# Kernel optimization log

Hardware: AMD Instinct MI355X
Metric: run time of the kernel (lower is better)

The kernel has to match this reference:

```python
import jax, jax.numpy as jnp
import numpy as np

N_HEAD = 16  # head_dim = C // N_HEAD = 128


def setup_inputs() -> dict:
    key = jax.random.key(0)
    k1, k2, k3 = jax.random.split(key, 3)
    B, T, C = 2, 2048, 2048
    x = jax.random.normal(k1, (B, T, C), dtype=jnp.float32)
    # c_attn: Linear(C, 3*C), no bias; stored as (in, out) for x @ W
    w_attn = jax.random.normal(k2, (C, 3 * C), dtype=jnp.float32) * (1.0 / np.sqrt(C))
    # c_proj: Linear(C, C), no bias
    w_proj = jax.random.normal(k3, (C, C), dtype=jnp.float32) * (1.0 / np.sqrt(C))
    return {"x": x, "w_attn": w_attn, "w_proj": w_proj}


def reference(x, w_attn, w_proj):
    B, T, C = x.shape
    H = N_HEAD
    D = C // H  # head dimension
    qkv = x @ w_attn                      # [B, T, 3C]
    q, k, v = jnp.split(qkv, 3, axis=-1)  # each [B, T, C]
    # [B, T, C] -> [B, H, T, D]
    q = q.reshape(B, T, H, D).transpose(0, 2, 1, 3)
    k = k.reshape(B, T, H, D).transpose(0, 2, 1, 3)
    v = v.reshape(B, T, H, D).transpose(0, 2, 1, 3)
    scale = 1.0 / np.sqrt(D).astype(np.float32)
    att = jnp.einsum('bhqd,bhkd->bhqk', q, k) * scale  # [B, H, T, T]
    causal = jnp.tril(jnp.ones((T, T), dtype=bool))
    att = jnp.where(causal[None, None, :, :], att, jnp.float32(-jnp.inf))
    att = jax.nn.softmax(att, axis=-1)
    y = jnp.einsum('bhqk,bhkd->bhqd', att, v)  # [B, H, T, D]
    y = y.transpose(0, 2, 1, 3).reshape(B, T, C)
    # all_reduce is identity with number_of_workers=1; dropout=0 (eval)
    return y @ w_proj
```

## Files before the change

### kernel.cpp

```cpp
#include <hip/hip_runtime.h>
#include <hip/hip_bf16.h>
#include <stdint.h>

#define TLEN 2048
#define CDIM 2048
#define BDIM 2
#define HDIM 16
#define DHEAD 128
#define QROW ((size_t)(2 * CDIM))

typedef __bf16 bf16x8 __attribute__((ext_vector_type(8)));
typedef float f32x4 __attribute__((ext_vector_type(4)));

__device__ __forceinline__ uint16_t f32_to_bf16(float f) {
    uint32_t u = __builtin_bit_cast(uint32_t, f);
    uint32_t r = (u + 0x7FFFu + ((u >> 16) & 1u)) >> 16;
    return (uint16_t)r;
}
__device__ __forceinline__ float bf16_to_f32(uint32_t h) {
    uint32_t u = h << 16;
    return __builtin_bit_cast(float, u);
}

__device__ __forceinline__ void gload_lds16(const uint16_t* g, uint16_t* l) {
    __builtin_amdgcn_global_load_lds(
        (const __attribute__((address_space(1))) uint32_t*)g,
        (__attribute__((address_space(3))) uint32_t*)l, 16, 0, 0);
}

__global__ void cvt_f32_bf16(const float* __restrict__ in, uint16_t* __restrict__ out, int n) {
    int i = (blockIdx.x * blockDim.x + threadIdx.x) * 4;
    if (i + 3 < n) {
        float4 f = *reinterpret_cast<const float4*>(in + i);
        ushort4 o;
        o.x = f32_to_bf16(f.x);
        o.y = f32_to_bf16(f.y);
        o.z = f32_to_bf16(f.z);
        o.w = f32_to_bf16(f.w);
        *reinterpret_cast<ushort4*>(out + i) = o;
    }
}

__global__ __launch_bounds__(256) void transpose_cvt(const float* __restrict__ in,
                                                     uint16_t* __restrict__ out,
                                                     int R, int Cc) {
    __shared__ uint16_t tile[64][65];
    int c0 = blockIdx.x * 64;
    int r0 = blockIdx.y * 64;
    int tc = threadIdx.x & 63;
    int t4 = threadIdx.x >> 6;
    for (int rr = t4; rr < 64; rr += 4) {
        tile[rr][tc] = f32_to_bf16(in[(size_t)(r0 + rr) * Cc + c0 + tc]);
    }
    __syncthreads();
    int wr = threadIdx.x & 63;
    for (int cc = t4; cc < 64; cc += 4) {
        out[(size_t)(c0 + cc) * R + r0 + wr] = tile[wr][cc];
    }
}


#define RD8(P, OFF) (*reinterpret_cast<const bf16x8*>((P) + (OFF)))

#define PH_RDA(BA, MB)                                              \
    _Pragma("unroll") for (int mi = 0; mi < 4; mi++) {              \
        af[mi][0] = RD8(BA, rdAo + ((MB) + mi) * 1024 + kblk0);     \
        af[mi][1] = RD8(BA, rdAo + ((MB) + mi) * 1024 + kblk1);     \
    }

#define PH_RDB(BB, NIB)                                                  \
    _Pragma("unroll") for (int ni = 0; ni < 2; ni++) {                   \
        bf[(NIB) + ni][0] = RD8(BB, rdBo + ((NIB) + ni) * 1024 + kblk0); \
        bf[(NIB) + ni][1] = RD8(BB, rdBo + ((NIB) + ni) * 1024 + kblk1); \
    }

#define PH_MFMA(MB, NIB)                                                        \
    __builtin_amdgcn_s_barrier();                                               \
    asm volatile("s_waitcnt lgkmcnt(0)" ::: "memory");                          \
    __builtin_amdgcn_s_setprio(1);                                              \
    _Pragma("unroll") for (int mi = 0; mi < 4; mi++)                            \
    _Pragma("unroll") for (int ni = 0; ni < 2; ni++) {                          \
        acc[(MB) + mi][(NIB) + ni] = __builtin_amdgcn_mfma_f32_16x16x32_bf16(   \
            af[mi][0], bf[(NIB) + ni][0], acc[(MB) + mi][(NIB) + ni], 0, 0, 0); \
        acc[(MB) + mi][(NIB) + ni] = __builtin_amdgcn_mfma_f32_16x16x32_bf16(   \
            af[mi][1], bf[(NIB) + ni][1], acc[(MB) + mi][(NIB) + ni], 0, 0, 0); \
    }                                                                           \
    __builtin_amdgcn_s_setprio(0);                                              \
    __builtin_amdgcn_s_barrier();                                               \
    __builtin_amdgcn_sched_barrier(0);

#define TILE(S, T)                                           \
    {                                                        \
        const int k0 = (T) * 64;                             \
        const uint16_t* bA = As + ((S) + wrow) * 8192;       \
        const uint16_t* bB = Bs + ((S) + bsel) * 8192;       \
        PH_RDA(bA, 0)                                        \
        PH_RDB(bB, 0)                                        \
        PH_MFMA(0, 0)                                        \
        PH_RDB(bB, 2)                                        \
        PH_MFMA(0, 2)                                        \
        PH_RDA(bA, 4)                                        \
        if ((T) + 2 < nt) {                                  \
            stB((S), 0, k0 + 128);                           \
            stB((S), 1, k0 + 128);                           \
        }                                                    \
        PH_MFMA(4, 2)                                        \
        if ((T) + 2 < nt) {                                  \
            stA((S), 0, k0 + 128);                           \
            stA((S), 1, k0 + 128);                           \
            asm volatile("s_waitcnt vmcnt(8)" ::: "memory"); \
        } else {                                             \
            asm volatile("s_waitcnt vmcnt(0)" ::: "memory"); \
        }                                                    \
        PH_MFMA(4, 0)                                        \
    }

template <int MODE>
__global__ __launch_bounds__(512, 2) void gemm_bf16_256(const uint16_t* __restrict__ A,
                                                        const uint16_t* __restrict__ Bt,
                                                        void* __restrict__ Cp,
                                                        uint16_t* __restrict__ vt,
                                                        int M, int N, int K, int xm) {
    __shared__ __align__(16) uint16_t lds[65536];
    uint16_t* const As = lds;
    uint16_t* const Bs = lds + 32768;

    const int tid = threadIdx.x;
    const int wave = tid >> 6;
    const int lane = tid & 63;
    const int l15 = lane & 15;
    const int quad = lane >> 4;
    const int wrow = wave >> 2;
    const int wcol = wave & 3;
    const int bsel = wcol >> 1;

    const int gm = gridDim.y, gn = gridDim.x;
    const int flat = blockIdx.y * gn + blockIdx.x;
    const int xcd = flat & 7;
    const int j = flat >> 3;
    const int xn = 8 / xm;
    const int RM = gm / xm;
    const int RN = gn / xn;
    const int m_blk = (xcd / xn) * RM + (j % RM);
    const int n_blk = (xcd % xn) * RN + (j / RM);
    const int m0 = m_blk * 256;
    const int n0 = n_blk * 256;

    const int srow = wave * 8 + (lane >> 3);
    const int scol = ((lane & 7) ^ (lane >> 3)) * 8;
    const uint16_t* Ag = A + (size_t)(m0 + srow) * K + scol;
    const uint16_t* Bg = Bt + (size_t)(n0 + srow) * K + scol;
    const int ldsoff = wave * 512;

    const int rdAo = l15 * 64;
    const int rdBo = ((wcol & 1) * 64 + l15) * 64;
    const int kblk0 = (quad ^ (l15 & 7)) * 8;
    const int kblk1 = ((4 + quad) ^ (l15 & 7)) * 8;

    const int nt = K >> 6;
    f32x4 acc[8][4] = {};
    bf16x8 af[4][2], bf[4][2];

    auto stA = [&](int sb, int h, int kk) {
        const uint16_t* s = Ag + (size_t)(h * 128) * K + kk;
        uint16_t* d = As + (sb + h) * 8192 + ldsoff;
        gload_lds16(s, d);
        gload_lds16(s + (size_t)64 * K, d + 4096);
    };
    auto stB = [&](int sb, int h, int kk) {
        const uint16_t* s = Bg + (size_t)(h * 128) * K + kk;
        uint16_t* d = Bs + (sb + h) * 8192 + ldsoff;
        gload_lds16(s, d);
        gload_lds16(s + (size_t)64 * K, d + 4096);
    };

    stB(0, 0, 0);
    stB(0, 1, 0);
    stA(0, 0, 0);
    stA(0, 1, 0);
    stB(2, 0, 64);
    stB(2, 1, 64);
    stA(2, 0, 64);
    stA(2, 1, 64);
    asm volatile("s_waitcnt vmcnt(8)" ::: "memory");
    __builtin_amdgcn_s_barrier();
    __builtin_amdgcn_sched_barrier(0);

    for (int t = 0; t < nt; t += 2) {
        TILE(0, t)
        TILE(2, t + 1)
    }

    const bool vmode = (MODE == 2) && (n0 >= 2 * CDIM);
#pragma unroll
    for (int mi = 0; mi < 8; mi++)
#pragma unroll
        for (int ni = 0; ni < 4; ni++) {
            if (vmode) {
                int col = n0 + wcol * 64 + ni * 16 + l15;
                int vcol = col - 2 * CDIM;
                int hh = vcol >> 7, d = vcol & 127;
                int rowm = m0 + wrow * 128 + mi * 16 + quad * 4;
                int bb = rowm >> 11, tt = rowm & 2047;
                uint32_t lo = (uint32_t)f32_to_bf16(acc[mi][ni][0]) |
                              ((uint32_t)f32_to_bf16(acc[mi][ni][1]) << 16);
                uint32_t hi = (uint32_t)f32_to_bf16(acc[mi][ni][2]) |
                              ((uint32_t)f32_to_bf16(acc[mi][ni][3]) << 16);
                *reinterpret_cast<uint2*>(
                    vt + ((size_t)((bb * HDIM + hh) * DHEAD + d)) * TLEN + tt) =
                    make_uint2(lo, hi);
            } else {
#pragma unroll
                for (int r = 0; r < 4; r++) {
                    int row = m0 + wrow * 128 + mi * 16 + quad * 4 + r;
                    int col = n0 + wcol * 64 + ni * 16 + l15;
                    float v = acc[mi][ni][r];
                    if (MODE == 2)
                        ((uint16_t*)Cp)[(size_t)row * (2 * CDIM) + col] = f32_to_bf16(v);
                    else if (MODE == 1)
                        ((uint16_t*)Cp)[(size_t)row * N + col] = f32_to_bf16(v);
                    else
                        ((float*)Cp)[(size_t)row * N + col] = v;
                }
            }
        }
}

#define ATT_C1 0.12751743f
#define ATT_C2 17.3123405f

__global__ __launch_bounds__(256) void attn_mfma3(const uint16_t* __restrict__ qkv,
                                                  const uint16_t* __restrict__ vtg,
                                                  uint16_t* __restrict__ y) {
    __shared__ __align__(16) uint16_t Ks[64 * 128];
    __shared__ __align__(16) uint16_t Vts[128 * 64];
    __shared__ __align__(16) uint16_t Ps[4][32 * 72];

    const int tid = threadIdx.x;
    const int wave = tid >> 6;
    const int lane = tid & 63;
    const int l15 = lane & 15;
    const int quad = lane >> 4;
    const int h = blockIdx.y;
    const int b = blockIdx.z;
    const int qblk = (int)gridDim.x - 1 - (int)blockIdx.x;
    const int qbase = qblk * 128 + wave * 32;
    const int kmax = qbase + 31;

    const uint16_t* kg = qkv + (size_t)b * TLEN * QROW + CDIM + h * DHEAD;
    const uint16_t* vg = vtg + (size_t)(b * HDIM + h) * DHEAD * TLEN;
    uint16_t* PsW = Ps[wave];

    int koff[4], voff[4];
#pragma unroll
    for (int i = 0; i < 4; i++) {
        int Lb = (wave * 4 + i) * 64 + lane;
        int key = Lb >> 4;
        int ck = (Lb & 15) ^ (key & 15);
        koff[i] = key * (int)QROW + ck * 8;
        int d = Lb >> 3;
        int cv = (Lb & 7) ^ (d & 7);
        voff[i] = d * TLEN + cv * 8;
    }

    bf16x8 qfrag[2][4];
#pragma unroll
    for (int m = 0; m < 2; m++) {
        const uint16_t* qp =
            qkv + (size_t)(b * TLEN + qbase + m * 16 + l15) * QROW + h * DHEAD + quad * 8;
#pragma unroll
        for (int kc = 0; kc < 4; kc++)
            qfrag[m][kc] = *reinterpret_cast<const bf16x8*>(qp + kc * 32);
    }

    f32x4 oacc[2][8] = {};
    float psum[2] = {0.f, 0.f};

    const int diagT = qblk * 2 + (wave >> 1);
    const int ntiles = qblk * 2 + 2;

    for (int t = 0; t < ntiles; t++) {
        const int j0 = t * 64;
        if (t > 0) __syncthreads();
        {
            const uint16_t* kj = kg + (size_t)j0 * QROW;
            const uint16_t* vj = vg + j0;
#pragma unroll
            for (int i = 0; i < 4; i++) {
                gload_lds16(kj + koff[i], Ks + (wave * 4 + i) * 512);
                gload_lds16(vj + voff[i], Vts + (wave * 4 + i) * 512);
            }
        }
        __syncthreads();
        if (t > diagT) continue;

        const bool masked = (t == diagT);
        const int n0max = masked ? ((kmax - j0) >> 4) : 3;

        f32x4 st[4][2];
#pragma unroll
        for (int n0 = 0; n0 < 4; n0++) {
            if (masked && n0 > n0max) continue;
            bf16x8 kf[4];
#pragma unroll
            for (int kc = 0; kc < 4; kc++) {
                int cpr = (kc * 4 + quad) ^ l15;
                kf[kc] = *reinterpret_cast<const bf16x8*>(
                    Ks + (n0 * 16 + l15) * 128 + cpr * 8);
            }
#pragma unroll
            for (int m = 0; m < 2; m++) {
                f32x4 acc = {};
#pragma unroll
                for (int kc = 0; kc < 4; kc++)
                    acc = __builtin_amdgcn_mfma_f32_16x16x32_bf16(
                        kf[kc], qfrag[m][kc], acc, 0, 0, 0);
                st[n0][m] = acc;
            }
        }

#pragma unroll
        for (int n0 = 0; n0 < 4; n0++) {
            if (masked && n0 > n0max) continue;
#pragma unroll
            for (int m = 0; m < 2; m++) {
                uint32_t pk0, pk1;
                float pv[4];
#pragma unroll
                for (int r = 0; r < 4; r++) {
                    float p = exp2f(st[n0][m][r] * ATT_C1 - ATT_C2);
                    if (masked) {
                        int key = j0 + n0 * 16 + quad * 4 + r;
                        int q = qbase + m * 16 + l15;
                        if (key > q) p = 0.f;
                    }
                    uint32_t pb = f32_to_bf16(p);
                    pv[r] = bf16_to_f32(pb);
                    if (r == 0) pk0 = pb;
                    else if (r == 1) pk0 |= pb << 16;
                    else if (r == 2) pk1 = pb;
                    else pk1 |= pb << 16;
                }
                psum[m] += (pv[0] + pv[1]) + (pv[2] + pv[3]);
                *reinterpret_cast<uint2*>(PsW + (m * 16 + l15) * 72 + n0 * 16 + quad * 4) =
                    make_uint2(pk0, pk1);
            }
        }

        const int kcend = masked ? (((kmax - j0) >> 5) + 1) : 2;
#pragma unroll
        for (int kc = 0; kc < 2; kc++) {
            if (kc >= kcend) continue;
            bf16x8 pf[2];
#pragma unroll
            for (int m = 0; m < 2; m++)
                pf[m] = *reinterpret_cast<const bf16x8*>(
                    PsW + (m * 16 + l15) * 72 + kc * 32 + quad * 8);
#pragma unroll
            for (int n0 = 0; n0 < 8; n0++) {
                int cpr = (kc * 4 + quad) ^ (l15 & 7);
                bf16x8 vf = *reinterpret_cast<const bf16x8*>(
                    Vts + (n0 * 16 + l15) * 64 + cpr * 8);
#pragma unroll
                for (int m = 0; m < 2; m++)
                    oacc[m][n0] = __builtin_amdgcn_mfma_f32_16x16x32_bf16(
                        pf[m], vf, oacc[m][n0], 0, 0, 0);
            }
        }
    }

#pragma unroll
    for (int m = 0; m < 2; m++) {
        float s = psum[m];
        s += __shfl_xor(s, 16);
        s += __shfl_xor(s, 32);
        psum[m] = 1.0f / s;
    }
    uint16_t* ybase = y + (size_t)(b * TLEN + qbase) * CDIM + h * DHEAD;
#pragma unroll
    for (int m = 0; m < 2; m++)
#pragma unroll
        for (int r = 0; r < 4; r++) {
            float inv = __shfl(psum[m], quad * 4 + r);
#pragma unroll
            for (int n0 = 0; n0 < 8; n0++)
                ybase[(size_t)(m * 16 + quad * 4 + r) * CDIM + n0 * 16 + l15] =
                    f32_to_bf16(oacc[m][n0][r] * inv);
        }
}

extern "C" void kernel_launch(void* const* d_in, const int* in_sizes, int n_in,
                              void* d_out, int out_size, void* d_ws, size_t ws_size,
                              hipStream_t stream) {
    const float* x = (const float*)d_in[0];
    const float* w_attn = (const float*)d_in[1];
    const float* w_proj = (const float*)d_in[2];
    float* out = (float*)d_out;

    const int M = BDIM * TLEN;
    const int K = CDIM;
    const int N3 = 3 * CDIM;

    char* ws = (char*)d_ws;
    uint16_t* xb = (uint16_t*)(ws);
    uint16_t* waT = (uint16_t*)(ws + 16777216);
    uint16_t* wpT = (uint16_t*)(ws + 41943040);
    uint16_t* qkp = (uint16_t*)(ws + 50331648);
    uint16_t* vtb = (uint16_t*)(ws + 83886080);
    uint16_t* yb = (uint16_t*)(ws + 100663296);

    cvt_f32_bf16<<<(M * K / 4 + 255) / 256, 256, 0, stream>>>(x, xb, M * K);
    transpose_cvt<<<dim3(N3 / 64, K / 64), 256, 0, stream>>>(w_attn, waT, K, N3);
    transpose_cvt<<<dim3(K / 64, K / 64), 256, 0, stream>>>(w_proj, wpT, K, K);
    gemm_bf16_256<2><<<dim3(N3 / 256, M / 256), 512, 0, stream>>>(xb, waT, (void*)qkp, vtb, M, N3, K, 2);
    attn_mfma3<<<dim3(TLEN / 128, HDIM, BDIM), 256, 0, stream>>>(qkp, vtb, yb);
    gemm_bf16_256<0><<<dim3(K / 256, M / 256), 512, 0, stream>>>(yb, wpT, (void*)out, nullptr, M, K, K, 4);
}
```

Before: 434.8 us.

## Software-pipeline LDS fragment reads across GEMM tile phases with double-buffered registers

Splits the A and B fragment registers into separate low/high and ping-pong buffers so that LDS reads for the next phase, and for the next k-tile, are issued before the current MFMA block runs. Partial lgkmcnt waits replace full drains, so LDS latency can overlap with matrix math. The global-load wait is also moved so that next-tile fragments can be read early. This raises register pressure and makes the waitcnt accounting fragile under a 512-thread, 2-blocks-per-CU launch bound.

```diff
diff --git a/kernel.cpp b/kernel.cpp
--- a/kernel.cpp
+++ b/kernel.cpp
@@ -62,57 +62,76 @@
 
 #define RD8(P, OFF) (*reinterpret_cast<const bf16x8*>((P) + (OFF)))
 
-#define PH_RDA(BA, MB)                                              \
-    _Pragma("unroll") for (int mi = 0; mi < 4; mi++) {              \
-        af[mi][0] = RD8(BA, rdAo + ((MB) + mi) * 1024 + kblk0);     \
-        af[mi][1] = RD8(BA, rdAo + ((MB) + mi) * 1024 + kblk1);     \
-    }
-
-#define PH_RDB(BB, NIB)                                                  \
-    _Pragma("unroll") for (int ni = 0; ni < 2; ni++) {                   \
-        bf[(NIB) + ni][0] = RD8(BB, rdBo + ((NIB) + ni) * 1024 + kblk0); \
-        bf[(NIB) + ni][1] = RD8(BB, rdBo + ((NIB) + ni) * 1024 + kblk1); \
-    }
-
-#define PH_MFMA(MB, NIB)                                                        \
-    __builtin_amdgcn_s_barrier();                                               \
-    asm volatile("s_waitcnt lgkmcnt(0)" ::: "memory");                          \
-    __builtin_amdgcn_s_setprio(1);                                              \
-    _Pragma("unroll") for (int mi = 0; mi < 4; mi++)                            \
-    _Pragma("unroll") for (int ni = 0; ni < 2; ni++) {                          \
-        acc[(MB) + mi][(NIB) + ni] = __builtin_amdgcn_mfma_f32_16x16x32_bf16(   \
-            af[mi][0], bf[(NIB) + ni][0], acc[(MB) + mi][(NIB) + ni], 0, 0, 0); \
-        acc[(MB) + mi][(NIB) + ni] = __builtin_amdgcn_mfma_f32_16x16x32_bf16(   \
-            af[mi][1], bf[(NIB) + ni][1], acc[(MB) + mi][(NIB) + ni], 0, 0, 0); \
-    }                                                                           \
-    __builtin_amdgcn_s_setprio(0);                                              \
-    __builtin_amdgcn_s_barrier();                                               \
+#define RDA(DST, P, MB)                                         \
+    _Pragma("unroll") for (int mi = 0; mi < 4; mi++) {          \
+        DST[mi][0] = RD8(P, rdAo + ((MB) + mi) * 1024 + kblk0); \
+        DST[mi][1] = RD8(P, rdAo + ((MB) + mi) * 1024 + kblk1); \
+    }
+
+#define RDB(DST, P, NB)                                         \
+    _Pragma("unroll") for (int ni = 0; ni < 2; ni++) {          \
+        DST[ni][0] = RD8(P, rdBo + ((NB) + ni) * 1024 + kblk0); \
+        DST[ni][1] = RD8(P, rdBo + ((NB) + ni) * 1024 + kblk1); \
+    }
+
+#define MFMA8(AF, BF, MB, NIB)                                                \
+    _Pragma("unroll") for (int mi = 0; mi < 4; mi++)                          \
+    _Pragma("unroll") for (int ni = 0; ni < 2; ni++) {                        \
+        acc[(MB) + mi][(NIB) + ni] = __builtin_amdgcn_mfma_f32_16x16x32_bf16( \
+            AF[mi][0], BF[ni][0], acc[(MB) + mi][(NIB) + ni], 0, 0, 0);       \
+        acc[(MB) + mi][(NIB) + ni] = __builtin_amdgcn_mfma_f32_16x16x32_bf16( \
+            AF[mi][1], BF[ni][1], acc[(MB) + mi][(NIB) + ni], 0, 0, 0);       \
+    }
+
+#define PHASE(LGN, AF, BF, MB, NIB)                           \
+    __builtin_amdgcn_s_barrier();                             \
+    asm volatile("s_waitcnt lgkmcnt(" #LGN ")" ::: "memory"); \
+    __builtin_amdgcn_sched_barrier(0);                        \
+    __builtin_amdgcn_s_setprio(1);                            \
+    MFMA8(AF, BF, MB, NIB)                                    \
+    __builtin_amdgcn_s_setprio(0);                            \
+    __builtin_amdgcn_s_barrier();                             \
     __builtin_amdgcn_sched_barrier(0);
 
-#define TILE(S, T)                                           \
-    {                                                        \
-        const int k0 = (T) * 64;                             \
-        const uint16_t* bA = As + ((S) + wrow) * 8192;       \
-        const uint16_t* bB = Bs + ((S) + bsel) * 8192;       \
-        PH_RDA(bA, 0)                                        \
-        PH_RDB(bB, 0)                                        \
-        PH_MFMA(0, 0)                                        \
-        PH_RDB(bB, 2)                                        \
-        PH_MFMA(0, 2)                                        \
-        PH_RDA(bA, 4)                                        \
-        if ((T) + 2 < nt) {                                  \
-            stB((S), 0, k0 + 128);                           \
-            stB((S), 1, k0 + 128);                           \
-        }                                                    \
-        PH_MFMA(4, 2)                                        \
-        if ((T) + 2 < nt) {                                  \
-            stA((S), 0, k0 + 128);                           \
-            stA((S), 1, k0 + 128);                           \
-            asm volatile("s_waitcnt vmcnt(8)" ::: "memory"); \
-        } else {                                             \
-            asm volatile("s_waitcnt vmcnt(0)" ::: "memory"); \
-        }                                                    \
-        PH_MFMA(4, 0)                                        \
+#define TILE(S, T, BFL, BFH)                                  \
+    {                                                         \
+        const int k0 = (T) * 64;                              \
+        const uint16_t* pA = As + ((S) + wrow) * 8192;        \
+        const uint16_t* pB = Bs + ((S) + bsel) * 8192;        \
+        const uint16_t* pAn = As + (((S) ^ 2) + wrow) * 8192; \
+        const uint16_t* pBn = Bs + (((S) ^ 2) + bsel) * 8192; \
+                               \
+        RDB(BFH, pB, 2)                                       \
+        PHASE(4, aL, BFL, 0, 0)                               \
+                               \
+        RDA(aH, pA, 4)                                        \
+        PHASE(8, aL, BFH, 0, 2)                               \
+                               \
+        if ((T) + 2 < nt) {                                   \
+            stB((S), 0, k0 + 128);                            \
+            stB((S), 1, k0 + 128);                            \
+        }                                                     \
+        PHASE(0, aH, BFH, 4, 2)                               \
+          \
+        if ((T) + 2 < nt) {                                   \
+            asm volatile("s_waitcnt vmcnt(4)" ::: "memory");  \
+            stA((S), 0, k0 + 128);                            \
+            stA((S), 1, k0 + 128);                            \
+        } else if ((T) + 1 < nt) {                            \
+            asm volatile("s_waitcnt vmcnt(0)" ::: "memory");  \
+        }                                                     \
+        __builtin_amdgcn_s_barrier();                         \
+        if ((T) + 1 < nt) {                                   \
+            RDA(aL, pAn, 0)                                   \
+            RDB(BFH, pBn, 0)                                  \
+        }                                                     \
+        asm volatile("s_waitcnt lgkmcnt(12)" ::: "memory");   \
+        __builtin_amdgcn_sched_barrier(0);                    \
+        __builtin_amdgcn_s_setprio(1);                        \
+        MFMA8(aH, BFL, 4, 0)                                  \
+        __builtin_amdgcn_s_setprio(0);                        \
+        __builtin_amdgcn_s_barrier();                         \
+        __builtin_amdgcn_sched_barrier(0);                    \
     }
 
 template <int MODE>
@@ -159,7 +178,7 @@
 
     const int nt = K >> 6;
     f32x4 acc[8][4] = {};
-    bf16x8 af[4][2], bf[4][2];
+    bf16x8 aL[4][2], aH[4][2], b0[2][2], b1[2][2];
 
     auto stA = [&](int sb, int h, int kk) {
         const uint16_t* s = Ag + (size_t)(h * 128) * K + kk;
@@ -185,10 +204,12 @@
     asm volatile("s_waitcnt vmcnt(8)" ::: "memory");
     __builtin_amdgcn_s_barrier();
     __builtin_amdgcn_sched_barrier(0);
+    RDA(aL, (As + wrow * 8192), 0)
+    RDB(b0, (Bs + bsel * 8192), 0)
 
     for (int t = 0; t < nt; t += 2) {
-        TILE(0, t)
-        TILE(2, t + 1)
+        TILE(0, t, b0, b1)
+        TILE(2, t + 1, b1, b0)
     }
 
     const bool vmode = (MODE == 2) && (n0 >= 2 * CDIM);
```

After: 599.6 us. +37.9%, slower.

## Restructure GEMM tile schedule into two larger MFMA phases with fewer barriers

Applied to the files above, without the earlier changes.

Replaces the four-phase per-tile schedule, each phase with its own barrier pair and lgkmcnt(0) wait, with a two-phase schedule. All four B fragments are loaded once per tile and each phase issues 32 MFMAs over two A row groups, with the global-to-LDS prefetch stores issued between barriers. The goal is to cut barrier and LDS-wait overhead and to hand the matrix cores longer uninterrupted runs. In exchange the changed wait counts and barrier placement must still prevent LDS read/write races, and the final tile skips its vmcnt wait.

```diff
diff --git a/kernel.cpp b/kernel.cpp
--- a/kernel.cpp
+++ b/kernel.cpp
@@ -62,57 +62,61 @@
 
 #define RD8(P, OFF) (*reinterpret_cast<const bf16x8*>((P) + (OFF)))
 
-#define PH_RDA(BA, MB)                                              \
-    _Pragma("unroll") for (int mi = 0; mi < 4; mi++) {              \
-        af[mi][0] = RD8(BA, rdAo + ((MB) + mi) * 1024 + kblk0);     \
-        af[mi][1] = RD8(BA, rdAo + ((MB) + mi) * 1024 + kblk1);     \
-    }
-
-#define PH_RDB(BB, NIB)                                                  \
-    _Pragma("unroll") for (int ni = 0; ni < 2; ni++) {                   \
-        bf[(NIB) + ni][0] = RD8(BB, rdBo + ((NIB) + ni) * 1024 + kblk0); \
-        bf[(NIB) + ni][1] = RD8(BB, rdBo + ((NIB) + ni) * 1024 + kblk1); \
-    }
-
-#define PH_MFMA(MB, NIB)                                                        \
-    __builtin_amdgcn_s_barrier();                                               \
-    asm volatile("s_waitcnt lgkmcnt(0)" ::: "memory");                          \
-    __builtin_amdgcn_s_setprio(1);                                              \
-    _Pragma("unroll") for (int mi = 0; mi < 4; mi++)                            \
-    _Pragma("unroll") for (int ni = 0; ni < 2; ni++) {                          \
-        acc[(MB) + mi][(NIB) + ni] = __builtin_amdgcn_mfma_f32_16x16x32_bf16(   \
-            af[mi][0], bf[(NIB) + ni][0], acc[(MB) + mi][(NIB) + ni], 0, 0, 0); \
-        acc[(MB) + mi][(NIB) + ni] = __builtin_amdgcn_mfma_f32_16x16x32_bf16(   \
-            af[mi][1], bf[(NIB) + ni][1], acc[(MB) + mi][(NIB) + ni], 0, 0, 0); \
-    }                                                                           \
-    __builtin_amdgcn_s_setprio(0);                                              \
-    __builtin_amdgcn_s_barrier();                                               \
-    __builtin_amdgcn_sched_barrier(0);
+#define RDA(DST, P, MB)                                         \
+    _Pragma("unroll") for (int mi = 0; mi < 4; mi++) {          \
+        DST[mi][0] = RD8(P, rdAo + ((MB) + mi) * 1024 + kblk0); \
+        DST[mi][1] = RD8(P, rdAo + ((MB) + mi) * 1024 + kblk1); \
+    }
+
+#define RDB4(DST, P)                                        \
+    _Pragma("unroll") for (int ni = 0; ni < 4; ni++) {      \
+        DST[ni][0] = RD8(P, rdBo + ni * 1024 + kblk0);      \
+        DST[ni][1] = RD8(P, rdBo + ni * 1024 + kblk1);      \
+    }
+
+#define MFMA32(MB)                                                    \
+    _Pragma("unroll") for (int kk = 0; kk < 2; kk++)                  \
+    _Pragma("unroll") for (int mi = 0; mi < 4; mi++)                  \
+    _Pragma("unroll") for (int ni = 0; ni < 4; ni++)                  \
+        acc[(MB) + mi][ni] = __builtin_amdgcn_mfma_f32_16x16x32_bf16( \
+            aA[mi][kk], bB[ni][kk], acc[(MB) + mi][ni], 0, 0, 0);
 
 #define TILE(S, T)                                           \
     {                                                        \
         const int k0 = (T) * 64;                             \
-        const uint16_t* bA = As + ((S) + wrow) * 8192;       \
-        const uint16_t* bB = Bs + ((S) + bsel) * 8192;       \
-        PH_RDA(bA, 0)                                        \
-        PH_RDB(bB, 0)                                        \
-        PH_MFMA(0, 0)                                        \
-        PH_RDB(bB, 2)                                        \
-        PH_MFMA(0, 2)                                        \
-        PH_RDA(bA, 4)                                        \
+        const uint16_t* pA = As + ((S) + wrow) * 8192;       \
+        const uint16_t* pB = Bs + ((S) + bsel) * 8192;       \
+        RDB4(bB, pB)                                         \
+        RDA(aA, pA, 0)                                       \
+        asm volatile("s_waitcnt lgkmcnt(8)" ::: "memory");   \
+        __builtin_amdgcn_s_barrier();      \
         if ((T) + 2 < nt) {                                  \
             stB((S), 0, k0 + 128);                           \
             stB((S), 1, k0 + 128);                           \
         }                                                    \
-        PH_MFMA(4, 2)                                        \
+        asm volatile("s_waitcnt lgkmcnt(0)" ::: "memory");   \
+        __builtin_amdgcn_sched_barrier(0);                   \
+        __builtin_amdgcn_s_setprio(1);                       \
+        MFMA32(0)                                            \
+        __builtin_amdgcn_s_setprio(0);                       \
+        RDA(aA, pA, 4)                                       \
+        asm volatile("s_waitcnt lgkmcnt(0)" ::: "memory");   \
+        __builtin_amdgcn_s_barrier();      \
         if ((T) + 2 < nt) {                                  \
             stA((S), 0, k0 + 128);                           \
             stA((S), 1, k0 + 128);                           \
+        }                                                    \
+        __builtin_amdgcn_sched_barrier(0);                   \
+        __builtin_amdgcn_s_setprio(1);                       \
+        MFMA32(4)                                            \
+        __builtin_amdgcn_s_setprio(0);                       \
+        if ((T) + 2 < nt) {                                  \
             asm volatile("s_waitcnt vmcnt(8)" ::: "memory"); \
-        } else {                                             \
+        } else if ((T) + 1 < nt) {                           \
             asm volatile("s_waitcnt vmcnt(0)" ::: "memory"); \
         }                                                    \
-        PH_MFMA(4, 0)                                        \
+        __builtin_amdgcn_s_barrier();       \
+        __builtin_amdgcn_sched_barrier(0);                   \
     }
 
 template <int MODE>
@@ -159,7 +163,7 @@
 
     const int nt = K >> 6;
     f32x4 acc[8][4] = {};
-    bf16x8 af[4][2], bf[4][2];
+    bf16x8 aA[4][2], bB[4][2];
 
     auto stA = [&](int sb, int h, int kk) {
         const uint16_t* s = Ag + (size_t)(h * 128) * K + kk;
```

Result: no change. 428.6 us (-1.4%).
